# Kernel optimization log

Hardware: AMD Instinct MI355X
Metric: run time of the kernel (lower is better)

Reference implementation:

```python
import jax, jax.numpy as jnp
import numpy as np

N_GRAPHS = 16
NODES_PER = 420
N = N_GRAPHS * NODES_PER      # 6720 nodes
DEG = 8
E = N * DEG                   # 53760 edges
HEADS = 2
IN_DIM = 2048
H1 = 1024                     # conv1 out per head
H2 = 64                       # conv2 out (heads=1)
OUT_DIM = 18
SCALE = 0.02


def _lin(x, W, b):
    return x @ W + b


def _transformer_conv(x, src, dst, Wq, bq, Wk, bk, Wv, bv, Ws, bs, heads, d):
    # PyG TransformerConv: per-edge dot-product attention, softmax over incoming
    # edges of each destination node, scatter-sum of messages, + root skip.
    n = x.shape[0]
    q = _lin(x, Wq, bq).reshape(n, heads, d)
    k = _lin(x, Wk, bk).reshape(n, heads, d)
    v = _lin(x, Wv, bv).reshape(n, heads, d)
    alpha = (q[dst] * k[src]).sum(-1) / jnp.sqrt(jnp.asarray(d, x.dtype))  # [E, heads]
    amax = jax.ops.segment_max(alpha, dst, num_segments=n)
    ex = jnp.exp(alpha - amax[dst])
    denom = jax.ops.segment_sum(ex, dst, num_segments=n)
    a = ex / (denom[dst] + 1e-16)
    out = jax.ops.segment_sum(v[src] * a[..., None], dst, num_segments=n)  # [N, heads, d]
    return out.reshape(n, heads * d) + _lin(x, Ws, bs)


def setup_inputs() -> dict:
    key = jax.random.key(0)
    ks = jax.random.split(key, 32)
    x = jax.random.normal(ks[0], (N, IN_DIM), dtype=jnp.float32)
    dst = jax.random.randint(ks[1], (E,), 0, N)
    # keep edges within each 420-node graph
    src = (dst // NODES_PER) * NODES_PER + jax.random.randint(ks[2], (E,), 0, NODES_PER)
    edge_index = jnp.stack([src, dst]).astype(jnp.int64)  # [2, E]
    connectivity = jax.random.randint(ks[3], (N,), 1, 6).astype(jnp.int64)  # lobes 1..5
    p = lambda i, shape: SCALE * jax.random.normal(ks[i], shape, dtype=jnp.float32)
    inp = {
        'x': x, 'edge_index': edge_index, 'connectivity': connectivity,
        'node_pe': p(4, (NODES_PER, IN_DIM)),
        'lobe_pe': p(5, (5, IN_DIM)),
        'lung_pe': p(6, (2, IN_DIM)),
        'Wq1': p(7, (IN_DIM, HEADS * H1)), 'bq1': jnp.zeros((HEADS * H1,), jnp.float32),
        'Wk1': p(8, (IN_DIM, HEADS * H1)), 'bk1': jnp.zeros((HEADS * H1,), jnp.float32),
        'Wv1': p(9, (IN_DIM, HEADS * H1)), 'bv1': jnp.zeros((HEADS * H1,), jnp.float32),
        'Ws1': p(10, (IN_DIM, HEADS * H1)), 'bs1': jnp.zeros((HEADS * H1,), jnp.float32),
        'Wq2': p(11, (HEADS * H1, H2)), 'bq2': jnp.zeros((H2,), jnp.float32),
        'Wk2': p(12, (HEADS * H1, H2)), 'bk2': jnp.zeros((H2,), jnp.float32),
        'Wv2': p(13, (HEADS * H1, H2)), 'bv2': jnp.zeros((H2,), jnp.float32),
        'Ws2': p(14, (HEADS * H1, H2)), 'bs2': jnp.zeros((H2,), jnp.float32),
        'W_fc1': p(15, (NODES_PER * H2, 256)), 'b_fc1': jnp.zeros((256,), jnp.float32),
        'W_fc2': p(16, (256, 128)), 'b_fc2': jnp.zeros((128,), jnp.float32),
        'W_fc3': p(17, (128, 64)), 'b_fc3': jnp.zeros((64,), jnp.float32),
        'W_fc4': p(18, (64, OUT_DIM)), 'b_fc4': jnp.zeros((OUT_DIM,), jnp.float32),
    }
    return inp


def reference(x, edge_index, connectivity, node_pe, lobe_pe, lung_pe,
              Wq1, bq1, Wk1, bk1, Wv1, bv1, Ws1, bs1,
              Wq2, bq2, Wk2, bk2, Wv2, bv2, Ws2, bs2,
              W_fc1, b_fc1, W_fc2, b_fc2, W_fc3, b_fc3, W_fc4, b_fc4):
    src, dst = edge_index[0], edge_index[1]
    # positional embeddings: node PE tiled per graph, lobe PE (conn in 1..5),
    # lung PE (lobes 1,2 -> lung 0; lobes 3,4,5 -> lung 1)
    h = x + jnp.tile(node_pe, (N_GRAPHS, 1))
    h = h + lobe_pe[connectivity - 1]
    h = h + lung_pe[jnp.where(connectivity <= 2, 0, 1)]
    h = jax.nn.relu(_transformer_conv(h, src, dst, Wq1, bq1, Wk1, bk1, Wv1, bv1, Ws1, bs1, HEADS, H1))
    h = jax.nn.relu(_transformer_conv(h, src, dst, Wq2, bq2, Wk2, bk2, Wv2, bv2, Ws2, bs2, 1, H2))
    h = h.reshape(-1, NODES_PER * H2)  # [B, 420*64]
    h = jax.nn.relu(_lin(h, W_fc1, b_fc1))
    h = jax.nn.relu(_lin(h, W_fc2, b_fc2))
    h = jax.nn.relu(_lin(h, W_fc3, b_fc3))
    return _lin(h, W_fc4, b_fc4)
```

## Files before the change

### kernel.cpp

```cpp
#include <hip/hip_runtime.h>
#include <stdint.h>

#define N_GRAPHS 16
#define NODES_PER 420
#define NN (N_GRAPHS * NODES_PER)
#define MP 6784
#define EE (NN * 8)
#define IN_DIM 2048
#define NCAT1 8192
#define NCAT2 256
#define KDIM 2048

typedef __bf16 bf16x8 __attribute__((ext_vector_type(8)));
typedef float f32x4 __attribute__((ext_vector_type(4)));
typedef unsigned short u16x8 __attribute__((ext_vector_type(8)));

__device__ __forceinline__ unsigned short f2bf(float f) {
  unsigned u = __float_as_uint(f);
  u += 0x7FFFu + ((u >> 16) & 1u);
  return (unsigned short)(u >> 16);
}
__device__ __forceinline__ float bf2f(unsigned short h) {
  return __uint_as_float(((unsigned)h) << 16);
}

__device__ __forceinline__ void gl2lds16(const void* g, const void* l) {
  __builtin_amdgcn_global_load_lds(
      (const __attribute__((address_space(1))) void*)(uintptr_t)g,
      (__attribute__((address_space(3))) void*)(unsigned int)(uintptr_t)l,
      16, 0, 0);
}

__global__ void prep_k(int* cnt, float* bcat1, float* bcat2, float* f1,
                       const float* bq1, const float* bk1, const float* bv1, const float* bs1,
                       const float* bq2, const float* bk2, const float* bv2, const float* bs2,
                       const float* bfc1) {
  int i = blockIdx.x * 256 + threadIdx.x;
  if (i < NN) cnt[i] = 0;
  if (i < NCAT1) {
    const float* p = i < 2048 ? bq1 : i < 4096 ? bk1 : i < 6144 ? bv1 : bs1;
    bcat1[i] = p[i & 2047];
  }
  if (i < NCAT2) {
    const float* p = i < 64 ? bq2 : i < 128 ? bk2 : i < 192 ? bv2 : bs2;
    bcat2[i] = p[i & 63];
  }
  if (i < 16 * 256) f1[i] = bfc1[i & 255];
}

__global__ void cnt_edges_k(const int* __restrict__ ei, int* __restrict__ cnt) {
  int e = blockIdx.x * 256 + threadIdx.x;
  if (e < EE) atomicAdd(&cnt[ei[EE + e]], 1);
}

__global__ void scan_offs_k(const int* __restrict__ cnt, int* __restrict__ offs,
                            int* __restrict__ cursor) {
  const int CH = 7;
  int t = threadIdx.x;
  int base = t * CH;
  int s = 0;
#pragma unroll
  for (int j = 0; j < CH; j++) { int idx = base + j; if (idx < NN) s += cnt[idx]; }
  __shared__ int sc[1024];
  sc[t] = s;
  __syncthreads();
  for (int d = 1; d < 1024; d <<= 1) {
    int v = 0;
    if (t >= d) v = sc[t - d];
    __syncthreads();
    if (t >= d) sc[t] += v;
    __syncthreads();
  }
  int run = sc[t] - s;
#pragma unroll
  for (int j = 0; j < CH; j++) {
    int idx = base + j;
    if (idx < NN) { offs[idx] = run; cursor[idx] = run; run += cnt[idx]; }
  }
  if (t == 1023) offs[NN] = run;
}

__global__ void scatter_k(const int* __restrict__ ei, int* __restrict__ cursor,
                          int* __restrict__ psrc) {
  int e = blockIdx.x * 256 + threadIdx.x;
  if (e < EE) {
    int d = ei[EE + e];
    int pos = atomicAdd(&cursor[d], 1);
    psrc[pos] = ei[e];
  }
}

__global__ void pe_add_k(const float* __restrict__ x, const int* __restrict__ conn,
                         const float* __restrict__ npe, const float* __restrict__ lpe,
                         const float* __restrict__ gpe, unsigned short* __restrict__ h0) {
  const int n = blockIdx.x, t = threadIdx.x;
  const int c = conn[n];
  const float4* x4 = (const float4*)(x + (size_t)n * IN_DIM);
  const float4* n4 = (const float4*)(npe + (size_t)(n % NODES_PER) * IN_DIM);
  const float4* l4 = (const float4*)(lpe + (size_t)(c - 1) * IN_DIM);
  const float4* g4 = (const float4*)(gpe + (size_t)(c <= 2 ? 0 : 1) * IN_DIM);
  ushort4* o4 = (ushort4*)(h0 + (size_t)n * IN_DIM);
#pragma unroll
  for (int i = 0; i < 2; i++) {
    int idx = i * 256 + t;
    float4 a = x4[idx], b = n4[idx], cc = l4[idx], d = g4[idx];
    ushort4 o;
    o.x = f2bf(a.x + b.x + cc.x + d.x);
    o.y = f2bf(a.y + b.y + cc.y + d.y);
    o.z = f2bf(a.z + b.z + cc.z + d.z);
    o.w = f2bf(a.w + b.w + cc.w + d.w);
    o4[idx] = o;
  }
}

__global__ void transw_k(const float* W0, const float* W1, const float* W2, const float* W3,
                         unsigned short* __restrict__ out, int K, int Ncol) {
  __shared__ float tile[32][33];
  const int z = blockIdx.z;
  const float* W = z == 0 ? W0 : z == 1 ? W1 : z == 2 ? W2 : W3;
  unsigned short* o = out + (size_t)z * Ncol * K;
  const int n0 = blockIdx.x * 32, k0 = blockIdx.y * 32;
  const int tx = threadIdx.x, ty = threadIdx.y;
#pragma unroll
  for (int r = 0; r < 4; r++)
    tile[ty + r * 8][tx] = W[(size_t)(k0 + ty + r * 8) * Ncol + n0 + tx];
  __syncthreads();
#pragma unroll
  for (int r = 0; r < 4; r++)
    o[(size_t)(n0 + ty + r * 8) * K + k0 + tx] = f2bf(tile[tx][ty + r * 8]);
}

template <int BM, int BN, int OUTF>
__launch_bounds__(256, 3)
__global__ void gemm_bt_k(const unsigned short* __restrict__ A,
                          const unsigned short* __restrict__ Bt,
                          const float* __restrict__ bias, void* __restrict__ C,
                          int Mblks, int Nsz, int K) {
  constexpr int BK = 32;
  constexpr int WTM = BM / 32, WTN = BN / 32;
  __shared__ __align__(16) unsigned short lA[BM * BK];
  __shared__ __align__(16) unsigned short lB[BN * BK];
  const int t = threadIdx.x;
  const int w = t >> 6, lane = t & 63;
  const int wm = w >> 1, wn = w & 1;
  const int quad = lane >> 4, l16 = lane & 15;

  const int NB = Nsz / BN;
  const int lin = blockIdx.x;
  const int stripe = lin / (8 * NB);
  const int rem = lin - stripe * 8 * NB;
  const int hh = min(8, Mblks - stripe * 8);
  const int mb = stripe * 8 + rem % hh;
  const int nb = rem / hh;
  const int m0 = mb * BM, n0 = nb * BN;

  f32x4 acc[WTM][WTN];
#pragma unroll
  for (int i = 0; i < WTM; i++)
#pragma unroll
    for (int j = 0; j < WTN; j++)
#pragma unroll
      for (int r = 0; r < 4; r++) acc[i][j][r] = 0.f;

  const int srow = t >> 2;
  const int scol = (((t & 3) ^ ((srow + (srow >> 2)) & 3)) * 8);
  const unsigned short* Ab = A + (size_t)(m0 + srow) * K + scol;
  const unsigned short* Bb = Bt + (size_t)(n0 + srow) * K + scol;

  for (int k0 = 0; k0 < K; k0 += BK) {
    __syncthreads();
#pragma unroll
    for (int r = 0; r < BM / 64; r++)
      gl2lds16(Ab + (size_t)r * 64 * K + k0, (const char*)lA + r * 4096 + t * 16);
#pragma unroll
    for (int r = 0; r < BN / 64; r++)
      gl2lds16(Bb + (size_t)r * 64 * K + k0, (const char*)lB + r * 4096 + t * 16);
    __syncthreads();

    bf16x8 afr[WTM], bfr[WTN];
#pragma unroll
    for (int i = 0; i < WTM; i++) {
      int row = wm * (BM / 2) + i * 16 + l16;
      int sw = quad ^ ((row + (row >> 2)) & 3);
      afr[i] = __builtin_bit_cast(bf16x8, *(const int4*)(&lA[row * 32 + sw * 8]));
    }
#pragma unroll
    for (int j = 0; j < WTN; j++) {
      int row = wn * (BN / 2) + j * 16 + l16;
      int sw = quad ^ ((row + (row >> 2)) & 3);
      bfr[j] = __builtin_bit_cast(bf16x8, *(const int4*)(&lB[row * 32 + sw * 8]));
    }
#pragma unroll
    for (int i = 0; i < WTM; i++)
#pragma unroll
      for (int j = 0; j < WTN; j++)
        acc[i][j] = __builtin_amdgcn_mfma_f32_16x16x32_bf16(afr[i], bfr[j], acc[i][j], 0, 0, 0);
  }

#pragma unroll
  for (int j = 0; j < WTN; j++) {
    const int col = n0 + wn * (BN / 2) + j * 16 + l16;
    const float bs = bias[col];
#pragma unroll
    for (int i = 0; i < WTM; i++) {
#pragma unroll
      for (int r = 0; r < 4; r++) {
        int row = m0 + wm * (BM / 2) + i * 16 + quad * 4 + r;
        float v = acc[i][j][r] + bs;
        if constexpr (OUTF)
          ((float*)C)[(size_t)row * Nsz + col] = v;
        else
          ((unsigned short*)C)[(size_t)row * Nsz + col] = f2bf(v);
      }
    }
  }
}

__global__ __launch_bounds__(256) void attn1_k(const unsigned short* __restrict__ qkvs,
                                               const int* __restrict__ offs,
                                               const int* __restrict__ psrc,
                                               unsigned short* __restrict__ h1) {
  const int bid = blockIdx.x;
  const int xcd = bid & 7, idx = bid >> 3;
  const int head = idx / 840;
  const int r2 = idx - head * 840;
  const int g = xcd * 2 + r2 / 420;
  const int n = g * 420 + r2 % 420;
  const int t = threadIdx.x, w = t >> 6, lane = t & 63;
  __shared__ __align__(16) unsigned short s_q[1024];
  __shared__ float s_al[64];
  __shared__ int s_src[64];
  __shared__ float s_m, s_l, s_sc;
  const size_t base = (size_t)n * NCAT1;
  const size_t ho = (size_t)head * 1024;
  *(ushort4*)(s_q + t * 4) = *(const ushort4*)(qkvs + base + ho + t * 4);
  float acc[4] = {0.f, 0.f, 0.f, 0.f};
  if (t == 0) { s_m = -1e30f; s_l = 0.f; }
  __syncthreads();
  const int e0 = offs[n], e1 = offs[n + 1];
  for (int c0 = e0; c0 < e1; c0 += 64) {
    const int ce = min(64, e1 - c0);
    if (t < ce) s_src[t] = psrc[c0 + t];
    __syncthreads();
    for (int e = w; e < ce; e += 4) {
      const unsigned short* kp = qkvs + (size_t)s_src[e] * NCAT1 + 2048 + ho;
      float p = 0.f;
#pragma unroll
      for (int i = 0; i < 2; i++) {
        u16x8 kv = *(const u16x8*)(kp + i * 512 + lane * 8);
        u16x8 qv = *(const u16x8*)(s_q + i * 512 + lane * 8);
#pragma unroll
        for (int j = 0; j < 8; j++) p += bf2f(qv[j]) * bf2f(kv[j]);
      }
#pragma unroll
      for (int s = 32; s > 0; s >>= 1) p += __shfl_xor(p, s, 64);
      if (lane == 0) s_al[e] = p * 0.03125f;
    }
    __syncthreads();
    if (t == 0) {
      float mo = s_m, mn = mo;
      for (int e = 0; e < ce; e++) mn = fmaxf(mn, s_al[e]);
      float sc = __expf(mo - mn);
      float l = s_l * sc;
      for (int e = 0; e < ce; e++) {
        float we = __expf(s_al[e] - mn);
        l += we;
        s_al[e] = we;
      }
      s_m = mn; s_l = l; s_sc = sc;
    }
    __syncthreads();
    const float sc = s_sc;
#pragma unroll
    for (int j = 0; j < 4; j++) acc[j] *= sc;
    for (int e = 0; e < ce; e++) {
      const unsigned short* vp = qkvs + (size_t)s_src[e] * NCAT1 + 4096 + ho;
      const float we = s_al[e];
      ushort4 vv = *(const ushort4*)(vp + t * 4);
      acc[0] += we * bf2f(vv.x);
      acc[1] += we * bf2f(vv.y);
      acc[2] += we * bf2f(vv.z);
      acc[3] += we * bf2f(vv.w);
    }
    __syncthreads();
  }
  const float inv = 1.f / (s_l + 1e-16f);
  ushort4 sk = *(const ushort4*)(qkvs + base + 6144 + ho + t * 4);
  ushort4 o;
  o.x = f2bf(fmaxf(acc[0] * inv + bf2f(sk.x), 0.f));
  o.y = f2bf(fmaxf(acc[1] * inv + bf2f(sk.y), 0.f));
  o.z = f2bf(fmaxf(acc[2] * inv + bf2f(sk.z), 0.f));
  o.w = f2bf(fmaxf(acc[3] * inv + bf2f(sk.w), 0.f));
  *(ushort4*)(h1 + (size_t)n * 2048 + ho + t * 4) = o;
}

__global__ __launch_bounds__(64) void attn2_k(const float* __restrict__ qkvs2,
                                              const int* __restrict__ offs,
                                              const int* __restrict__ psrc,
                                              float* __restrict__ h2) {
  const int bid = blockIdx.x;
  const int xcd = bid & 7, idx = bid >> 3;
  const int g = xcd * 2 + idx / 420;
  const int n = g * 420 + idx % 420;
  const int t = threadIdx.x;
  const size_t rb = (size_t)n * NCAT2;
  const float q = qkvs2[rb + t];
  float m = -1e30f, l = 0.f, acc = 0.f;
  const int e0 = offs[n], e1 = offs[n + 1];
  for (int e = e0; e < e1; e++) {
    const int src = psrc[e];
    float p = q * qkvs2[(size_t)src * NCAT2 + 64 + t];
#pragma unroll
    for (int s = 32; s > 0; s >>= 1) p += __shfl_xor(p, s, 64);
    p *= 0.125f;
    const float mn = fmaxf(m, p);
    const float sc = __expf(m - mn), we = __expf(p - mn);
    const float v = qkvs2[(size_t)src * NCAT2 + 128 + t];
    l = l * sc + we;
    acc = acc * sc + we * v;
    m = mn;
  }
  float o = acc / (l + 1e-16f) + qkvs2[rb + 192 + t];
  h2[(size_t)n * 64 + t] = fmaxf(o, 0.f);
}

__global__ __launch_bounds__(256) void fc1_k(const float* __restrict__ h2,
                                             const float* __restrict__ W,
                                             float* __restrict__ f1) {
  __shared__ float sA[16][256];
  const int t = threadIdx.x, k0 = blockIdx.x * 256;
#pragma unroll
  for (int r = 0; r < 16; r++) sA[r][t] = h2[(size_t)r * 26880 + k0 + t];
  __syncthreads();
  float acc[16];
#pragma unroll
  for (int r = 0; r < 16; r++) acc[r] = 0.f;
  for (int kk = 0; kk < 256; kk++) {
    const float wv = W[(size_t)(k0 + kk) * 256 + t];
#pragma unroll
    for (int r = 0; r < 16; r++) acc[r] += sA[r][kk] * wv;
  }
#pragma unroll
  for (int r = 0; r < 16; r++) atomicAdd(&f1[r * 256 + t], acc[r]);
}

__global__ __launch_bounds__(128) void fc234_k(const float* __restrict__ f1,
                                               const float* __restrict__ W2, const float* __restrict__ b2,
                                               const float* __restrict__ W3, const float* __restrict__ b3,
                                               const float* __restrict__ W4, const float* __restrict__ b4,
                                               float* __restrict__ out) {
  const int row = blockIdx.x, t = threadIdx.x;
  __shared__ float s2[128], s3[64];
  float acc = 0.f;
  for (int k = 0; k < 256; k++) acc += fmaxf(f1[row * 256 + k], 0.f) * W2[k * 128 + t];
  s2[t] = fmaxf(acc + b2[t], 0.f);
  __syncthreads();
  if (t < 64) {
    float a3 = 0.f;
    for (int k = 0; k < 128; k++) a3 += s2[k] * W3[k * 64 + t];
    s3[t] = fmaxf(a3 + b3[t], 0.f);
  }
  __syncthreads();
  if (t < 18) {
    float a4 = 0.f;
    for (int k = 0; k < 64; k++) a4 += s3[k] * W4[k * 18 + t];
    out[row * 18 + t] = a4 + b4[t];
  }
}

extern "C" void kernel_launch(void* const* d_in, const int* in_sizes, int n_in,
                              void* d_out, int out_size, void* d_ws, size_t ws_size,
                              hipStream_t stream) {
  const float* x    = (const float*)d_in[0];
  const int*   ei   = (const int*)d_in[1];
  const int*   conn = (const int*)d_in[2];
  const float* npe  = (const float*)d_in[3];
  const float* lpe  = (const float*)d_in[4];
  const float* gpe  = (const float*)d_in[5];
  const float* Wq1 = (const float*)d_in[6];  const float* bq1 = (const float*)d_in[7];
  const float* Wk1 = (const float*)d_in[8];  const float* bk1 = (const float*)d_in[9];
  const float* Wv1 = (const float*)d_in[10]; const float* bv1 = (const float*)d_in[11];
  const float* Ws1 = (const float*)d_in[12]; const float* bs1 = (const float*)d_in[13];
  const float* Wq2 = (const float*)d_in[14]; const float* bq2 = (const float*)d_in[15];
  const float* Wk2 = (const float*)d_in[16]; const float* bk2 = (const float*)d_in[17];
  const float* Wv2 = (const float*)d_in[18]; const float* bv2 = (const float*)d_in[19];
  const float* Ws2 = (const float*)d_in[20]; const float* bs2 = (const float*)d_in[21];
  const float* Wf1 = (const float*)d_in[22]; const float* bf1 = (const float*)d_in[23];
  const float* Wf2 = (const float*)d_in[24]; const float* bf2 = (const float*)d_in[25];
  const float* Wf3 = (const float*)d_in[26]; const float* bf3 = (const float*)d_in[27];
  const float* Wf4 = (const float*)d_in[28]; const float* bf4 = (const float*)d_in[29];
  float* out = (float*)d_out;

  char* ws = (char*)d_ws;
  size_t off = 0;
  auto alloc = [&](size_t bytes) -> void* {
    void* p = ws + off;
    off += (bytes + 255) & ~(size_t)255;
    return p;
  };
  unsigned short* h0    = (unsigned short*)alloc((size_t)MP * IN_DIM * 2);
  unsigned short* w1t   = (unsigned short*)alloc((size_t)NCAT1 * KDIM * 2);
  unsigned short* qkvs1 = (unsigned short*)alloc((size_t)MP * NCAT1 * 2);
  unsigned short* w2t   = (unsigned short*)alloc((size_t)NCAT2 * KDIM * 2);
  float* qkvs2 = (float*)alloc((size_t)MP * NCAT2 * 4);
  float* h2    = (float*)alloc((size_t)NN * 64 * 4);
  float* bcat1 = (float*)alloc(NCAT1 * 4);
  float* bcat2 = (float*)alloc(NCAT2 * 4);
  float* f1    = (float*)alloc(16 * 256 * 4);
  int* cnt    = (int*)alloc(NN * 4);
  int* offs   = (int*)alloc((NN + 1) * 4);
  int* cursor = (int*)alloc(NN * 4);
  int* psrc   = (int*)alloc(EE * 4);
  unsigned short* h1 = w1t;

  prep_k<<<32, 256, 0, stream>>>(cnt, bcat1, bcat2, f1,
                                 bq1, bk1, bv1, bs1, bq2, bk2, bv2, bs2, bf1);
  cnt_edges_k<<<EE / 256, 256, 0, stream>>>(ei, cnt);
  scan_offs_k<<<1, 1024, 0, stream>>>(cnt, offs, cursor);
  scatter_k<<<EE / 256, 256, 0, stream>>>(ei, cursor, psrc);
  pe_add_k<<<NN, 256, 0, stream>>>(x, conn, npe, lpe, gpe, h0);
  transw_k<<<dim3(64, 64, 4), dim3(32, 8), 0, stream>>>(Wq1, Wk1, Wv1, Ws1, w1t, KDIM, 2048);
  transw_k<<<dim3(2, 64, 4), dim3(32, 8), 0, stream>>>(Wq2, Wk2, Wv2, Ws2, w2t, KDIM, 64);
  gemm_bt_k<128, 128, 0><<<(MP / 128) * (NCAT1 / 128), 256, 0, stream>>>(
      h0, w1t, bcat1, qkvs1, MP / 128, NCAT1, KDIM);
  attn1_k<<<2 * NN, 256, 0, stream>>>(qkvs1, offs, psrc, h1);
  gemm_bt_k<64, 64, 1><<<(MP / 64) * (NCAT2 / 64), 256, 0, stream>>>(
      h1, w2t, bcat2, qkvs2, MP / 64, NCAT2, KDIM);
  attn2_k<<<NN, 64, 0, stream>>>(qkvs2, offs, psrc, h2);
  fc1_k<<<26880 / 256, 256, 0, stream>>>(h2, Wf1, f1);
  fc234_k<<<16, 128, 0, stream>>>(f1, Wf2, bf2, Wf3, bf3, Wf4, bf4, out);
}
```

Baseline: 661.2 us.

## Deepen GEMM K-tile, split-K the second projection, and merge setup launches

The bf16 GEMM now stages a 64-wide K slice per iteration with an 8-slot XOR swizzle, which halves the number of barrier-separated load phases. It also drops the grouped block-index remapping in favour of a plain 2D/3D grid. The layer-2 projection uses 4-way split-K with float atomicAdd into an output that pe_add_k now pre-fills with the biases. The two weight-transpose launches are merged into one grid, and the offset scan becomes a single-wave shuffle scan. The risks are worse L2 locality for the large GEMM without the stripe remap, and extra atomic traffic on the small GEMM.

```diff
diff --git a/kernel.cpp b/kernel.cpp
--- a/kernel.cpp
+++ b/kernel.cpp
@@ -31,9 +31,8 @@
       16, 0, 0);
 }
 
-__global__ void prep_k(int* cnt, float* bcat1, float* bcat2, float* f1,
+__global__ void prep_k(int* cnt, float* bcat1, float* f1,
                        const float* bq1, const float* bk1, const float* bv1, const float* bs1,
-                       const float* bq2, const float* bk2, const float* bv2, const float* bs2,
                        const float* bfc1) {
   int i = blockIdx.x * 256 + threadIdx.x;
   if (i < NN) cnt[i] = 0;
@@ -41,10 +40,6 @@
     const float* p = i < 2048 ? bq1 : i < 4096 ? bk1 : i < 6144 ? bv1 : bs1;
     bcat1[i] = p[i & 2047];
   }
-  if (i < NCAT2) {
-    const float* p = i < 64 ? bq2 : i < 128 ? bk2 : i < 192 ? bv2 : bs2;
-    bcat2[i] = p[i & 63];
-  }
   if (i < 16 * 256) f1[i] = bfc1[i & 255];
 }
 
@@ -53,31 +48,27 @@
   if (e < EE) atomicAdd(&cnt[ei[EE + e]], 1);
 }
 
-__global__ void scan_offs_k(const int* __restrict__ cnt, int* __restrict__ offs,
-                            int* __restrict__ cursor) {
-  const int CH = 7;
-  int t = threadIdx.x;
-  int base = t * CH;
+__global__ __launch_bounds__(64) void scan_offs_k(const int* __restrict__ cnt,
+                                                  int* __restrict__ offs,
+                                                  int* __restrict__ cursor) {
+  const int t = threadIdx.x;
+  const int base = t * 105;
   int s = 0;
-#pragma unroll
-  for (int j = 0; j < CH; j++) { int idx = base + j; if (idx < NN) s += cnt[idx]; }
-  __shared__ int sc[1024];
-  sc[t] = s;
-  __syncthreads();
-  for (int d = 1; d < 1024; d <<= 1) {
-    int v = 0;
-    if (t >= d) v = sc[t - d];
-    __syncthreads();
-    if (t >= d) sc[t] += v;
-    __syncthreads();
-  }
-  int run = sc[t] - s;
-#pragma unroll
-  for (int j = 0; j < CH; j++) {
+#pragma unroll 1
+  for (int j = 0; j < 105; j++) s += cnt[base + j];
+  int pfx = s;
+#pragma unroll
+  for (int d = 1; d < 64; d <<= 1) {
+    int v = __shfl_up(pfx, d, 64);
+    if (t >= d) pfx += v;
+  }
+  int run = pfx - s;
+#pragma unroll 1
+  for (int j = 0; j < 105; j++) {
     int idx = base + j;
-    if (idx < NN) { offs[idx] = run; cursor[idx] = run; run += cnt[idx]; }
-  }
-  if (t == 1023) offs[NN] = run;
+    offs[idx] = run; cursor[idx] = run; run += cnt[idx];
+  }
+  if (t == 63) offs[NN] = run;
 }
 
 __global__ void scatter_k(const int* __restrict__ ei, int* __restrict__ cursor,
@@ -92,7 +83,10 @@
 
 __global__ void pe_add_k(const float* __restrict__ x, const int* __restrict__ conn,
                          const float* __restrict__ npe, const float* __restrict__ lpe,
-                         const float* __restrict__ gpe, unsigned short* __restrict__ h0) {
+                         const float* __restrict__ gpe, unsigned short* __restrict__ h0,
+                         float* __restrict__ qkvs2,
+                         const float* __restrict__ bq2, const float* __restrict__ bk2,
+                         const float* __restrict__ bv2, const float* __restrict__ bs2) {
   const int n = blockIdx.x, t = threadIdx.x;
   const int c = conn[n];
   const float4* x4 = (const float4*)(x + (size_t)n * IN_DIM);
@@ -111,15 +105,30 @@
     o.w = f2bf(a.w + b.w + cc.w + d.w);
     o4[idx] = o;
   }
-}
-
-__global__ void transw_k(const float* W0, const float* W1, const float* W2, const float* W3,
-                         unsigned short* __restrict__ out, int K, int Ncol) {
+  const float* bp = t < 64 ? bq2 : t < 128 ? bk2 : t < 192 ? bv2 : bs2;
+  qkvs2[(size_t)n * NCAT2 + t] = bp[t & 63];
+}
+
+__global__ void transw_k(const float* Wq1, const float* Wk1, const float* Wv1, const float* Ws1,
+                         const float* Wq2, const float* Wk2, const float* Wv2, const float* Ws2,
+                         unsigned short* __restrict__ o1, unsigned short* __restrict__ o2) {
   __shared__ float tile[32][33];
   const int z = blockIdx.z;
-  const float* W = z == 0 ? W0 : z == 1 ? W1 : z == 2 ? W2 : W3;
-  unsigned short* o = out + (size_t)z * Ncol * K;
-  const int n0 = blockIdx.x * 32, k0 = blockIdx.y * 32;
+  const float* W;
+  unsigned short* o;
+  int n0, Ncol;
+  const int k0 = blockIdx.y * 32;
+  if (z < 4) {
+    W = z == 0 ? Wq1 : z == 1 ? Wk1 : z == 2 ? Wv1 : Ws1;
+    o = o1 + (size_t)z * 2048 * KDIM;
+    n0 = blockIdx.x * 32; Ncol = 2048;
+  } else {
+    if (blockIdx.x >= 8) return;
+    const int m = blockIdx.x >> 1;
+    W = m == 0 ? Wq2 : m == 1 ? Wk2 : m == 2 ? Wv2 : Ws2;
+    o = o2 + (size_t)m * 64 * KDIM;
+    n0 = (blockIdx.x & 1) * 32; Ncol = 64;
+  }
   const int tx = threadIdx.x, ty = threadIdx.y;
 #pragma unroll
   for (int r = 0; r < 4; r++)
@@ -127,7 +136,7 @@
   __syncthreads();
 #pragma unroll
   for (int r = 0; r < 4; r++)
-    o[(size_t)(n0 + ty + r * 8) * K + k0 + tx] = f2bf(tile[tx][ty + r * 8]);
+    o[(size_t)(n0 + ty + r * 8) * KDIM + k0 + tx] = f2bf(tile[tx][ty + r * 8]);
 }
 
 template <int BM, int BN, int OUTF>
@@ -135,24 +144,17 @@
 __global__ void gemm_bt_k(const unsigned short* __restrict__ A,
                           const unsigned short* __restrict__ Bt,
                           const float* __restrict__ bias, void* __restrict__ C,
-                          int Mblks, int Nsz, int K) {
-  constexpr int BK = 32;
+                          int Nsz, int K, int kIters) {
+  constexpr int BK = 64;
   constexpr int WTM = BM / 32, WTN = BN / 32;
+  constexpr int RA = BM / 32, RB = BN / 32;
   __shared__ __align__(16) unsigned short lA[BM * BK];
   __shared__ __align__(16) unsigned short lB[BN * BK];
   const int t = threadIdx.x;
   const int w = t >> 6, lane = t & 63;
   const int wm = w >> 1, wn = w & 1;
   const int quad = lane >> 4, l16 = lane & 15;
-
-  const int NB = Nsz / BN;
-  const int lin = blockIdx.x;
-  const int stripe = lin / (8 * NB);
-  const int rem = lin - stripe * 8 * NB;
-  const int hh = min(8, Mblks - stripe * 8);
-  const int mb = stripe * 8 + rem % hh;
-  const int nb = rem / hh;
-  const int m0 = mb * BM, n0 = nb * BN;
+  const int m0 = blockIdx.y * BM, n0 = blockIdx.x * BN;
 
   f32x4 acc[WTM][WTN];
 #pragma unroll
@@ -162,55 +164,58 @@
 #pragma unroll
       for (int r = 0; r < 4; r++) acc[i][j][r] = 0.f;
 
-  const int srow = t >> 2;
-  const int scol = (((t & 3) ^ ((srow + (srow >> 2)) & 3)) * 8);
-  const unsigned short* Ab = A + (size_t)(m0 + srow) * K + scol;
-  const unsigned short* Bb = Bt + (size_t)(n0 + srow) * K + scol;
-
-  for (int k0 = 0; k0 < K; k0 += BK) {
-    __syncthreads();
-#pragma unroll
-    for (int r = 0; r < BM / 64; r++)
-      gl2lds16(Ab + (size_t)r * 64 * K + k0, (const char*)lA + r * 4096 + t * 16);
-#pragma unroll
-    for (int r = 0; r < BN / 64; r++)
-      gl2lds16(Bb + (size_t)r * 64 * K + k0, (const char*)lB + r * 4096 + t * 16);
-    __syncthreads();
-
-    bf16x8 afr[WTM], bfr[WTN];
-#pragma unroll
-    for (int i = 0; i < WTM; i++) {
-      int row = wm * (BM / 2) + i * 16 + l16;
-      int sw = quad ^ ((row + (row >> 2)) & 3);
-      afr[i] = __builtin_bit_cast(bf16x8, *(const int4*)(&lA[row * 32 + sw * 8]));
+  const int srow = t >> 3;
+  const int scol = ((t & 7) ^ (srow & 7)) * 8;
+  const unsigned short* Ab = A + (size_t)(m0 + srow) * K + scol + blockIdx.z * (size_t)kIters * BK;
+  const unsigned short* Bb = Bt + (size_t)(n0 + srow) * K + scol + blockIdx.z * (size_t)kIters * BK;
+
+  for (int it = 0; it < kIters; it++) {
+    const int k0 = it * BK;
+    __syncthreads();
+#pragma unroll
+    for (int r = 0; r < RA; r++)
+      gl2lds16(Ab + (size_t)r * 32 * K + k0, (const char*)lA + r * 4096 + t * 16);
+#pragma unroll
+    for (int r = 0; r < RB; r++)
+      gl2lds16(Bb + (size_t)r * 32 * K + k0, (const char*)lB + r * 4096 + t * 16);
+    __syncthreads();
+
+#pragma unroll
+    for (int s = 0; s < 2; s++) {
+      bf16x8 afr[WTM], bfr[WTN];
+#pragma unroll
+      for (int i = 0; i < WTM; i++) {
+        int row = wm * (BM / 2) + i * 16 + l16;
+        int slot = (s * 4 + quad) ^ (row & 7);
+        afr[i] = __builtin_bit_cast(bf16x8, *(const int4*)(&lA[row * 64 + slot * 8]));
+      }
+#pragma unroll
+      for (int j = 0; j < WTN; j++) {
+        int row = wn * (BN / 2) + j * 16 + l16;
+        int slot = (s * 4 + quad) ^ (row & 7);
+        bfr[j] = __builtin_bit_cast(bf16x8, *(const int4*)(&lB[row * 64 + slot * 8]));
+      }
+#pragma unroll
+      for (int i = 0; i < WTM; i++)
+#pragma unroll
+        for (int j = 0; j < WTN; j++)
+          acc[i][j] = __builtin_amdgcn_mfma_f32_16x16x32_bf16(afr[i], bfr[j], acc[i][j], 0, 0, 0);
     }
-#pragma unroll
-    for (int j = 0; j < WTN; j++) {
-      int row = wn * (BN / 2) + j * 16 + l16;
-      int sw = quad ^ ((row + (row >> 2)) & 3);
-      bfr[j] = __builtin_bit_cast(bf16x8, *(const int4*)(&lB[row * 32 + sw * 8]));
-    }
-#pragma unroll
-    for (int i = 0; i < WTM; i++)
-#pragma unroll
-      for (int j = 0; j < WTN; j++)
-        acc[i][j] = __builtin_amdgcn_mfma_f32_16x16x32_bf16(afr[i], bfr[j], acc[i][j], 0, 0, 0);
   }
 
 #pragma unroll
   for (int j = 0; j < WTN; j++) {
     const int col = n0 + wn * (BN / 2) + j * 16 + l16;
-    const float bs = bias[col];
+    const float bs = OUTF ? 0.f : bias[col];
 #pragma unroll
     for (int i = 0; i < WTM; i++) {
 #pragma unroll
       for (int r = 0; r < 4; r++) {
         int row = m0 + wm * (BM / 2) + i * 16 + quad * 4 + r;
-        float v = acc[i][j][r] + bs;
         if constexpr (OUTF)
-          ((float*)C)[(size_t)row * Nsz + col] = v;
+          atomicAdd(&((float*)C)[(size_t)row * Nsz + col], acc[i][j][r]);
         else
-          ((unsigned short*)C)[(size_t)row * Nsz + col] = f2bf(v);
+          ((unsigned short*)C)[(size_t)row * Nsz + col] = f2bf(acc[i][j][r] + bs);
       }
     }
   }
@@ -405,7 +410,6 @@
   float* qkvs2 = (float*)alloc((size_t)MP * NCAT2 * 4);
   float* h2    = (float*)alloc((size_t)NN * 64 * 4);
   float* bcat1 = (float*)alloc(NCAT1 * 4);
-  float* bcat2 = (float*)alloc(NCAT2 * 4);
   float* f1    = (float*)alloc(16 * 256 * 4);
   int* cnt    = (int*)alloc(NN * 4);
   int* offs   = (int*)alloc((NN + 1) * 4);
@@ -413,19 +417,19 @@
   int* psrc   = (int*)alloc(EE * 4);
   unsigned short* h1 = w1t;
 
-  prep_k<<<32, 256, 0, stream>>>(cnt, bcat1, bcat2, f1,
-                                 bq1, bk1, bv1, bs1, bq2, bk2, bv2, bs2, bf1);
+  prep_k<<<32, 256, 0, stream>>>(cnt, bcat1, f1, bq1, bk1, bv1, bs1, bf1);
   cnt_edges_k<<<EE / 256, 256, 0, stream>>>(ei, cnt);
-  scan_offs_k<<<1, 1024, 0, stream>>>(cnt, offs, cursor);
+  scan_offs_k<<<1, 64, 0, stream>>>(cnt, offs, cursor);
   scatter_k<<<EE / 256, 256, 0, stream>>>(ei, cursor, psrc);
-  pe_add_k<<<NN, 256, 0, stream>>>(x, conn, npe, lpe, gpe, h0);
-  transw_k<<<dim3(64, 64, 4), dim3(32, 8), 0, stream>>>(Wq1, Wk1, Wv1, Ws1, w1t, KDIM, 2048);
-  transw_k<<<dim3(2, 64, 4), dim3(32, 8), 0, stream>>>(Wq2, Wk2, Wv2, Ws2, w2t, KDIM, 64);
-  gemm_bt_k<128, 128, 0><<<(MP / 128) * (NCAT1 / 128), 256, 0, stream>>>(
-      h0, w1t, bcat1, qkvs1, MP / 128, NCAT1, KDIM);
+  pe_add_k<<<NN, 256, 0, stream>>>(x, conn, npe, lpe, gpe, h0, qkvs2,
+                                   bq2, bk2, bv2, bs2);
+  transw_k<<<dim3(64, 64, 5), dim3(32, 8), 0, stream>>>(
+      Wq1, Wk1, Wv1, Ws1, Wq2, Wk2, Wv2, Ws2, w1t, w2t);
+  gemm_bt_k<128, 128, 0><<<dim3(NCAT1 / 128, MP / 128, 1), 256, 0, stream>>>(
+      h0, w1t, bcat1, qkvs1, NCAT1, KDIM, KDIM / 64);
   attn1_k<<<2 * NN, 256, 0, stream>>>(qkvs1, offs, psrc, h1);
-  gemm_bt_k<64, 64, 1><<<(MP / 64) * (NCAT2 / 64), 256, 0, stream>>>(
-      h1, w2t, bcat2, qkvs2, MP / 64, NCAT2, KDIM);
+  gemm_bt_k<64, 64, 1><<<dim3(NCAT2 / 64, MP / 64, 4), 256, 0, stream>>>(
+      h1, w2t, nullptr, qkvs2, NCAT2, KDIM, KDIM / 64 / 4);
   attn2_k<<<NN, 64, 0, stream>>>(qkvs2, offs, psrc, h2);
   fc1_k<<<26880 / 256, 256, 0, stream>>>(h2, Wf1, f1);
   fc234_k<<<16, 128, 0, stream>>>(f1, Wf2, bf2, Wf3, bf3, Wf4, bf4, out);
```

Measured after the change: 613.9 us. 7.2% less time.
